# Kernel tuning notes

Hardware: AMD Instinct MI355X
Metric: run time of the kernel (lower is better)

The kernel has to match this reference:

```python
import jax, jax.numpy as jnp
import numpy as np

NUM_HEADS = 16
KEY_SIZE = 64
HEAD_SIZE = 64


def setup_inputs() -> dict:
    key = jax.random.key(0)
    ks = jax.random.split(key, 8)
    B, S, D = 2, 2048, 1024
    s = 1.0 / np.sqrt(D)
    return {
        "q": jax.random.normal(ks[0], (B, S, D), jnp.float32),
        "k": jax.random.normal(ks[1], (B, S, D), jnp.float32),
        "v": jax.random.normal(ks[2], (B, S, D), jnp.float32),
        "v_mask": jax.random.randint(ks[3], (B, S), 0, 2, jnp.int32),
        "Wq": jax.random.normal(ks[4], (D, NUM_HEADS * KEY_SIZE), jnp.float32) * s,
        "Wk": jax.random.normal(ks[5], (D, NUM_HEADS * KEY_SIZE), jnp.float32) * s,
        "Wv": jax.random.normal(ks[6], (D, NUM_HEADS * HEAD_SIZE), jnp.float32) * s,
    }


def reference(q, k, v, v_mask, Wq, Wk, Wv):
    B, Sq, _ = q.shape
    Sk = k.shape[1]
    # projections + split heads: [B, S, H, d]
    qw = (q @ Wq).reshape(B, Sq, NUM_HEADS, KEY_SIZE)
    kw = (k @ Wk).reshape(B, Sk, NUM_HEADS, KEY_SIZE)
    vw = (v @ Wv).reshape(B, Sk, NUM_HEADS, HEAD_SIZE)
    # scores [B, H, Sq, Sk]
    a = jnp.einsum('bqhd,bkhd->bhqk', qw, kw) / np.sqrt(KEY_SIZE).astype(np.float32)
    # additive mask over key axis: x*m - (1-m)*1e12
    m = v_mask.astype(a.dtype)[:, None, None, :]
    a = a * m - (1.0 - m) * 1e12
    a = jax.nn.softmax(a, axis=-1)
    # output [B, Sq, H*head_size]
    o = jnp.einsum('bhqk,bkhd->bqhd', a, vw)
    return o.reshape(B, Sq, NUM_HEADS * HEAD_SIZE)
```

## Files before the change

kernel.cpp:

```cpp
#include <hip/hip_runtime.h>
#include <hip/hip_bf16.h>


#define SEQ 2048
#define DIM 1024
#define NPROJ 1024

typedef __bf16 bf16x8 __attribute__((ext_vector_type(8)));
typedef float floatx4 __attribute__((ext_vector_type(4)));
typedef float floatx16 __attribute__((ext_vector_type(16)));

__device__ inline unsigned short f2bf_bits(float x) {
  __hip_bfloat16 h = __float2bfloat16(x);
  return __builtin_bit_cast(unsigned short, h);
}

__device__ __forceinline__ void gload_lds16(const void* g, void* l) {
  __builtin_amdgcn_global_load_lds((const __attribute__((address_space(1))) void*)g,
                                   (__attribute__((address_space(3))) void*)l, 16, 0, 0);
}

__global__ __launch_bounds__(256) void cvt_x(
    const float* __restrict__ q, const float* __restrict__ k, const float* __restrict__ v,
    unsigned short* __restrict__ xb)
{
  const float* X = blockIdx.z == 0 ? q : (blockIdx.z == 1 ? k : v);
  unsigned short* O = xb + (size_t)blockIdx.z * 4096 * 1024;
  int i0 = blockIdx.x * 256 + threadIdx.x;
  #pragma unroll
  for (int it = 0; it < 4; ++it) {
    int i = i0 + it * 262144;
    float4 f = *reinterpret_cast<const float4*>(&X[(size_t)i * 4]);
    ushort4 o;
    o.x = f2bf_bits(f.x); o.y = f2bf_bits(f.y);
    o.z = f2bf_bits(f.z); o.w = f2bf_bits(f.w);
    *reinterpret_cast<ushort4*>(&O[(size_t)i * 4]) = o;
  }
}

__global__ __launch_bounds__(256) void transpose_w(
    const float* __restrict__ Wq, const float* __restrict__ Wk, const float* __restrict__ Wv,
    unsigned short* __restrict__ WqT, unsigned short* __restrict__ WkT, unsigned short* __restrict__ WvT)
{
  const float* W = blockIdx.z == 0 ? Wq : (blockIdx.z == 1 ? Wk : Wv);
  unsigned short* WT = blockIdx.z == 0 ? WqT : (blockIdx.z == 1 ? WkT : WvT);
  const float sc = (blockIdx.z == 0) ? 0.1803368801f : 1.0f;
  __shared__ float tile[64][65];
  const int k0 = blockIdx.x * 64;
  const int n0 = blockIdx.y * 64;
  const int t = threadIdx.x;
  #pragma unroll
  for (int it = 0; it < 4; ++it) {
    int idx = t + (it << 8);
    int r = idx >> 4, c4 = (idx & 15) << 2;
    float4 v = *reinterpret_cast<const float4*>(&W[(k0 + r) * DIM + n0 + c4]);
    tile[r][c4 + 0] = v.x; tile[r][c4 + 1] = v.y;
    tile[r][c4 + 2] = v.z; tile[r][c4 + 3] = v.w;
  }
  __syncthreads();
  #pragma unroll
  for (int it = 0; it < 4; ++it) {
    int idx = t + (it << 8);
    int r = idx >> 4, c4 = (idx & 15) << 2;
    ushort4 o;
    o.x = f2bf_bits(tile[c4 + 0][r] * sc);
    o.y = f2bf_bits(tile[c4 + 1][r] * sc);
    o.z = f2bf_bits(tile[c4 + 2][r] * sc);
    o.w = f2bf_bits(tile[c4 + 3][r] * sc);
    *reinterpret_cast<ushort4*>(&WT[(n0 + r) * DIM + k0 + c4]) = o;
  }
}

__global__ __launch_bounds__(256, 4) void proj_gemm(
    const unsigned short* __restrict__ xb,
    const unsigned short* __restrict__ WqT, const unsigned short* __restrict__ WkT,
    const unsigned short* __restrict__ WvT,
    unsigned short* __restrict__ qw, unsigned short* __restrict__ kw, unsigned short* __restrict__ vw)
{
  const unsigned short* X = xb + (size_t)blockIdx.z * 4096 * 1024;
  const unsigned short* WT = blockIdx.z == 0 ? WqT : (blockIdx.z == 1 ? WkT : WvT);
  unsigned short* Y = blockIdx.z == 0 ? qw : (blockIdx.z == 1 ? kw : vw);

  __shared__ unsigned short Al[2][128 * 32];
  __shared__ unsigned short Bl[2][128 * 32];

  const int m0 = blockIdx.x * 128, n0 = blockIdx.y * 128;
  const int t = threadIdx.x;
  const int lane = t & 63;
  const int wid = t >> 6;
  const int wm = (wid >> 1) << 6, wn = (wid & 1) << 6;
  const int qd = lane >> 4, ln = lane & 15;

  auto stage = [&](int ks, int bi) {
    const int kb = ks << 6;
    #pragma unroll
    for (int i = 0; i < 2; ++i) {
      int p = t + (i << 8);
      int r = p >> 2, c = p & 3;
      int f = (r + (r >> 2)) & 3;
      gload_lds16((const char*)X + (size_t)(m0 + r) * 2048 + kb + ((c ^ f) << 4),
                  (char*)&Al[bi][0] + p * 16);
      gload_lds16((const char*)WT + (size_t)(n0 + r) * 2048 + kb + ((c ^ f) << 4),
                  (char*)&Bl[bi][0] + p * 16);
    }
  };

  floatx4 acc[4][4] = {};
  stage(0, 0);

  for (int ks = 0; ks < 32; ++ks) {
    __syncthreads();
    if (ks + 1 < 32) stage(ks + 1, (ks + 1) & 1);
    const int bi = ks & 1;
    bf16x8 af[4], bfr[4];
    #pragma unroll
    for (int mb = 0; mb < 4; ++mb) {
      int m = wm + mb * 16 + ln;
      int fm = (m + (m >> 2)) & 3;
      af[mb] = *reinterpret_cast<const bf16x8*>(&Al[bi][m * 32 + ((qd ^ fm) << 3)]);
    }
    #pragma unroll
    for (int nb = 0; nb < 4; ++nb) {
      int n = wn + nb * 16 + ln;
      int fn = (n + (n >> 2)) & 3;
      bfr[nb] = *reinterpret_cast<const bf16x8*>(&Bl[bi][n * 32 + ((qd ^ fn) << 3)]);
    }
    #pragma unroll
    for (int mb = 0; mb < 4; ++mb)
      #pragma unroll
      for (int nb = 0; nb < 4; ++nb)
        acc[mb][nb] = __builtin_amdgcn_mfma_f32_16x16x32_bf16(af[mb], bfr[nb], acc[mb][nb], 0, 0, 0);
  }
  #pragma unroll
  for (int mb = 0; mb < 4; ++mb)
    #pragma unroll
    for (int nb = 0; nb < 4; ++nb)
      #pragma unroll
      for (int i = 0; i < 4; ++i) {
        int m = m0 + wm + mb * 16 + qd * 4 + i;
        int n = n0 + wn + nb * 16 + ln;
        Y[(size_t)m * NPROJ + n] = f2bf_bits(acc[mb][nb][i]);
      }
}

__global__ __launch_bounds__(256) void transpose_v(
    const unsigned short* __restrict__ vw, const int* __restrict__ vmask,
    unsigned short* __restrict__ vt, unsigned short* __restrict__ mb)
{
  if (blockIdx.y == 0 && blockIdx.x < 16) {
    int i = blockIdx.x * 256 + threadIdx.x;
    mb[i] = vmask[i] ? 0x3F80 : 0;
  }
  __shared__ unsigned short tile[64 * 64];
  const int t = threadIdx.x;
  const int s0 = blockIdx.x * 64;
  const int bh = blockIdx.y;
  const int b = bh >> 4, h = bh & 15;
  #pragma unroll
  for (int it = 0; it < 2; ++it) {
    int p = t + (it << 8);
    int s = p >> 3, c = p & 7;
    int cp = (c + (s >> 3) + (s & 7)) & 7;
    int4 d = *reinterpret_cast<const int4*>(&vw[(size_t)(b * SEQ + s0 + s) * NPROJ + h * 64 + c * 8]);
    if (vmask[b * SEQ + s0 + s] == 0) { d.x = 0; d.y = 0; d.z = 0; d.w = 0; }
    *reinterpret_cast<int4*>(&tile[s * 64 + cp * 8]) = d;
  }
  __syncthreads();
  #pragma unroll
  for (int it = 0; it < 2; ++it) {
    int d = (t >> 3) + (it << 5), sc = t & 7;
    struct { alignas(16) unsigned short u[8]; } o;
    #pragma unroll
    for (int j = 0; j < 8; ++j) {
      int s = sc * 8 + j;
      int cp = ((d >> 3) + (s >> 3) + (s & 7)) & 7;
      o.u[j] = tile[s * 64 + cp * 8 + (d & 7)];
    }
    *reinterpret_cast<int4*>(&vt[(size_t)(bh * 64 + d) * SEQ + s0 + sc * 8]) =
        *reinterpret_cast<const int4*>(o.u);
  }
}

__global__ __launch_bounds__(256, 2) void attn_fwd(
    const unsigned short* __restrict__ qw, const unsigned short* __restrict__ kw,
    const unsigned short* __restrict__ vt, const unsigned short* __restrict__ mb,
    float* __restrict__ out)
{
  extern __shared__ char smem[];
  unsigned short* Kl = (unsigned short*)smem;
  unsigned short* Vl = (unsigned short*)(smem + 16384);
  unsigned short* Ml = (unsigned short*)(smem + 32768);

  const int t = threadIdx.x, lane = t & 63, wid = t >> 6;
  const int l5 = lane & 31, hi = lane >> 5;
  const int bh = blockIdx.x;
  const int q0 = blockIdx.y * 128;
  const int b = bh >> 4, h = bh & 15;
  const int base = b * SEQ;
  const int wq = wid * 32;

  auto stage = [&](int kt, int bi) {
    const int k0 = kt << 6;
    #pragma unroll
    for (int i = 0; i < 2; ++i) {
      int rb = wid * 16 + i * 8;
      int r = rb + (lane >> 3);
      int rsrc = (r & ~12) | ((r & 4) << 1) | ((r & 8) >> 1);
      int sw = ((lane & 7) ^ (r & 7)) << 4;
      gload_lds16((const char*)kw + ((size_t)((base + k0 + rsrc) * NPROJ + h * 64) << 1) + sw,
                  (char*)&Kl[bi * 4096] + rb * 128);
      gload_lds16((const char*)vt + ((size_t)((bh * 64 + r) * SEQ + k0) << 1) + sw,
                  (char*)&Vl[bi * 4096] + rb * 128);
    }
    if (wid == 3 && lane < 8)
      gload_lds16((const char*)mb + ((size_t)(base + k0 + lane * 8) << 1), (char*)&Ml[bi * 64]);
  };

  bf16x8 qf[4];
  {
    const unsigned short* qptr =
        qw + (size_t)(base + q0 + wq + l5) * NPROJ + h * 64 + hi * 8;
    #pragma unroll
    for (int kk = 0; kk < 4; ++kk)
      qf[kk] = *reinterpret_cast<const bf16x8*>(qptr + kk * 16);
  }

  floatx16 oa0 = {}, oa1 = {}, la = {};
  stage(0, 0);

  #pragma unroll 2
  for (int kt = 0; kt < SEQ / 64; ++kt) {
    __syncthreads();
    if (kt + 1 < SEQ / 64) stage(kt + 1, (kt + 1) & 1);
    const int bi = kt & 1;

    floatx16 s0 = {}, s1 = {};
    #pragma unroll
    for (int kk = 0; kk < 4; ++kk) {
      int ph = ((kk * 2 + hi) ^ (l5 & 7)) << 3;
      bf16x8 k0f = *reinterpret_cast<const bf16x8*>(&Kl[bi * 4096 + l5 * 64 + ph]);
      bf16x8 k1f = *reinterpret_cast<const bf16x8*>(&Kl[bi * 4096 + (32 + l5) * 64 + ph]);
      s0 = __builtin_amdgcn_mfma_f32_32x32x16_bf16(k0f, qf[kk], s0, 0, 0, 0);
      s1 = __builtin_amdgcn_mfma_f32_32x32x16_bf16(k1f, qf[kk], s1, 0, 0, 0);
    }

    float pe[32];
    #pragma unroll
    for (int r = 0; r < 16; ++r) {
      pe[r]      = __builtin_amdgcn_exp2f(s0[r]);
      pe[16 + r] = __builtin_amdgcn_exp2f(s1[r]);
    }

    #pragma unroll
    for (int kk = 0; kk < 4; ++kk) {
      struct alignas(16) { unsigned short u[8]; } pk;
      #pragma unroll
      for (int j = 0; j < 8; ++j) pk.u[j] = f2bf_bits(pe[8 * kk + j]);
      bf16x8 pa = __builtin_bit_cast(bf16x8, pk);
      int ph = ((kk * 2 + hi) ^ (l5 & 7)) << 3;
      bf16x8 v0 = *reinterpret_cast<const bf16x8*>(&Vl[bi * 4096 + l5 * 64 + ph]);
      bf16x8 v1 = *reinterpret_cast<const bf16x8*>(&Vl[bi * 4096 + (32 + l5) * 64 + ph]);
      bf16x8 mf = *reinterpret_cast<const bf16x8*>(&Ml[bi * 64 + kk * 16 + hi * 8]);
      oa0 = __builtin_amdgcn_mfma_f32_32x32x16_bf16(pa, v0, oa0, 0, 0, 0);
      oa1 = __builtin_amdgcn_mfma_f32_32x32x16_bf16(pa, v1, oa1, 0, 0, 0);
      la  = __builtin_amdgcn_mfma_f32_32x32x16_bf16(pa, mf, la, 0, 0, 0);
    }
  }

  #pragma unroll
  for (int r = 0; r < 16; ++r) {
    int row = wq + (r & 3) + ((r >> 2) << 3) + (hi << 2);
    float inv = 1.0f / la[r];
    size_t o = (size_t)(base + q0 + row) * NPROJ + h * 64;
    out[o + l5] = oa0[r] * inv;
    out[o + 32 + l5] = oa1[r] * inv;
  }
}

extern "C" void kernel_launch(void* const* d_in, const int* in_sizes, int n_in,
                              void* d_out, int out_size, void* d_ws, size_t ws_size,
                              hipStream_t stream) {
  const float* q  = (const float*)d_in[0];
  const float* k  = (const float*)d_in[1];
  const float* v  = (const float*)d_in[2];
  const int* vm   = (const int*)d_in[3];
  const float* Wq = (const float*)d_in[4];
  const float* Wk = (const float*)d_in[5];
  const float* Wv = (const float*)d_in[6];
  float* out = (float*)d_out;

  unsigned short* ws = (unsigned short*)d_ws;
  unsigned short* WqT = ws + ((size_t)0 << 20);
  unsigned short* WkT = ws + ((size_t)1 << 20);
  unsigned short* WvT = ws + ((size_t)2 << 20);
  unsigned short* qw  = ws + ((size_t)3 << 20);
  unsigned short* kw  = ws + ((size_t)7 << 20);
  unsigned short* vw  = ws + ((size_t)11 << 20);
  unsigned short* xb  = ws + ((size_t)15 << 20);
  unsigned short* vt  = ws + ((size_t)15 << 20);
  unsigned short* mbv = WqT;

  cvt_x<<<dim3(1024, 1, 3), 256, 0, stream>>>(q, k, v, xb);
  transpose_w<<<dim3(16, 16, 3), 256, 0, stream>>>(Wq, Wk, Wv, WqT, WkT, WvT);
  proj_gemm<<<dim3(32, 8, 3), 256, 0, stream>>>(xb, WqT, WkT, WvT, qw, kw, vw);
  transpose_v<<<dim3(32, 32), 256, 0, stream>>>(vw, vm, vt, mbv);
  attn_fwd<<<dim3(32, 16), 256, 33024, stream>>>(qw, kw, vt, mbv, out);
}
```

Before: 101.4 us.

## Split key tiles across wave pairs in attention with LDS merge of partial outputs

The attention kernel grows from 4 to 8 waves per block. Each pair of waves shares a 32-query slice and splits each 64-key tile in half, computing half the scores and PV MFMAs per wave. Partial outputs and row sums are combined through shared memory at the end. s_setprio hints are added around the MFMA sections. This raises wave-level parallelism and latency hiding, at the cost of duplicated Q fragments, a final LDS reduction, and more register and occupancy pressure.

```diff
diff --git a/kernel.cpp b/kernel.cpp
--- a/kernel.cpp
+++ b/kernel.cpp
@@ -181,7 +181,7 @@
   }
 }
 
-__global__ __launch_bounds__(256, 2) void attn_fwd(
+__global__ __launch_bounds__(512, 4) void attn_fwd(
     const unsigned short* __restrict__ qw, const unsigned short* __restrict__ kw,
     const unsigned short* __restrict__ vt, const unsigned short* __restrict__ mb,
     float* __restrict__ out)
@@ -193,33 +193,30 @@
 
   const int t = threadIdx.x, lane = t & 63, wid = t >> 6;
   const int l5 = lane & 31, hi = lane >> 5;
+  const int qh = wid >> 1, kh = wid & 1;
   const int bh = blockIdx.x;
   const int q0 = blockIdx.y * 128;
   const int b = bh >> 4, h = bh & 15;
   const int base = b * SEQ;
-  const int wq = wid * 32;
 
   auto stage = [&](int kt, int bi) {
     const int k0 = kt << 6;
-    #pragma unroll
-    for (int i = 0; i < 2; ++i) {
-      int rb = wid * 16 + i * 8;
-      int r = rb + (lane >> 3);
-      int rsrc = (r & ~12) | ((r & 4) << 1) | ((r & 8) >> 1);
-      int sw = ((lane & 7) ^ (r & 7)) << 4;
-      gload_lds16((const char*)kw + ((size_t)((base + k0 + rsrc) * NPROJ + h * 64) << 1) + sw,
-                  (char*)&Kl[bi * 4096] + rb * 128);
-      gload_lds16((const char*)vt + ((size_t)((bh * 64 + r) * SEQ + k0) << 1) + sw,
-                  (char*)&Vl[bi * 4096] + rb * 128);
-    }
-    if (wid == 3 && lane < 8)
+    int rb = wid * 8;
+    int r = rb + (lane >> 3);
+    int rsrc = (r & ~12) | ((r & 4) << 1) | ((r & 8) >> 1);
+    int sw = ((lane & 7) ^ (r & 7)) << 4;
+    gload_lds16((const char*)kw + ((size_t)((base + k0 + rsrc) * NPROJ + h * 64) << 1) + sw,
+                (char*)&Kl[bi * 4096] + rb * 128);
+    gload_lds16((const char*)vt + ((size_t)((bh * 64 + r) * SEQ + k0) << 1) + sw,
+                (char*)&Vl[bi * 4096] + rb * 128);
+    if (wid == 7 && lane < 8)
       gload_lds16((const char*)mb + ((size_t)(base + k0 + lane * 8) << 1), (char*)&Ml[bi * 64]);
   };
 
   bf16x8 qf[4];
   {
     const unsigned short* qptr =
-        qw + (size_t)(base + q0 + wq + l5) * NPROJ + h * 64 + hi * 8;
+        qw + (size_t)(base + q0 + qh * 32 + l5) * NPROJ + h * 64 + hi * 8;
     #pragma unroll
     for (int kk = 0; kk < 4; ++kk)
       qf[kk] = *reinterpret_cast<const bf16x8*>(qptr + kk * 16);
@@ -234,46 +231,61 @@
     if (kt + 1 < SEQ / 64) stage(kt + 1, (kt + 1) & 1);
     const int bi = kt & 1;
 
-    floatx16 s0 = {}, s1 = {};
+    floatx16 s = {};
+    __builtin_amdgcn_s_setprio(1);
     #pragma unroll
     for (int kk = 0; kk < 4; ++kk) {
       int ph = ((kk * 2 + hi) ^ (l5 & 7)) << 3;
-      bf16x8 k0f = *reinterpret_cast<const bf16x8*>(&Kl[bi * 4096 + l5 * 64 + ph]);
-      bf16x8 k1f = *reinterpret_cast<const bf16x8*>(&Kl[bi * 4096 + (32 + l5) * 64 + ph]);
-      s0 = __builtin_amdgcn_mfma_f32_32x32x16_bf16(k0f, qf[kk], s0, 0, 0, 0);
-      s1 = __builtin_amdgcn_mfma_f32_32x32x16_bf16(k1f, qf[kk], s1, 0, 0, 0);
-    }
-
-    float pe[32];
-    #pragma unroll
-    for (int r = 0; r < 16; ++r) {
-      pe[r]      = __builtin_amdgcn_exp2f(s0[r]);
-      pe[16 + r] = __builtin_amdgcn_exp2f(s1[r]);
-    }
-
-    #pragma unroll
-    for (int kk = 0; kk < 4; ++kk) {
+      bf16x8 kf = *reinterpret_cast<const bf16x8*>(&Kl[bi * 4096 + (kh * 32 + l5) * 64 + ph]);
+      s = __builtin_amdgcn_mfma_f32_32x32x16_bf16(kf, qf[kk], s, 0, 0, 0);
+    }
+    __builtin_amdgcn_s_setprio(0);
+
+    float pe[16];
+    #pragma unroll
+    for (int r = 0; r < 16; ++r) pe[r] = __builtin_amdgcn_exp2f(s[r]);
+
+    #pragma unroll
+    for (int kk = 0; kk < 2; ++kk) {
       struct alignas(16) { unsigned short u[8]; } pk;
       #pragma unroll
       for (int j = 0; j < 8; ++j) pk.u[j] = f2bf_bits(pe[8 * kk + j]);
       bf16x8 pa = __builtin_bit_cast(bf16x8, pk);
-      int ph = ((kk * 2 + hi) ^ (l5 & 7)) << 3;
-      bf16x8 v0 = *reinterpret_cast<const bf16x8*>(&Vl[bi * 4096 + l5 * 64 + ph]);
-      bf16x8 v1 = *reinterpret_cast<const bf16x8*>(&Vl[bi * 4096 + (32 + l5) * 64 + ph]);
-      bf16x8 mf = *reinterpret_cast<const bf16x8*>(&Ml[bi * 64 + kk * 16 + hi * 8]);
+      int ch = ((4 * kh + 2 * kk + hi) ^ (l5 & 7)) << 3;
+      bf16x8 v0 = *reinterpret_cast<const bf16x8*>(&Vl[bi * 4096 + l5 * 64 + ch]);
+      bf16x8 v1 = *reinterpret_cast<const bf16x8*>(&Vl[bi * 4096 + (32 + l5) * 64 + ch]);
+      bf16x8 mf = *reinterpret_cast<const bf16x8*>(&Ml[bi * 64 + kh * 32 + kk * 16 + hi * 8]);
+      __builtin_amdgcn_s_setprio(1);
       oa0 = __builtin_amdgcn_mfma_f32_32x32x16_bf16(pa, v0, oa0, 0, 0, 0);
       oa1 = __builtin_amdgcn_mfma_f32_32x32x16_bf16(pa, v1, oa1, 0, 0, 0);
       la  = __builtin_amdgcn_mfma_f32_32x32x16_bf16(pa, mf, la, 0, 0, 0);
-    }
-  }
-
-  #pragma unroll
-  for (int r = 0; r < 16; ++r) {
-    int row = wq + (r & 3) + ((r >> 2) << 3) + (hi << 2);
-    float inv = 1.0f / la[r];
-    size_t o = (size_t)(base + q0 + row) * NPROJ + h * 64;
-    out[o + l5] = oa0[r] * inv;
-    out[o + 32 + l5] = oa1[r] * inv;
+      __builtin_amdgcn_s_setprio(0);
+    }
+  }
+
+  __syncthreads();
+  float* Mg = (float*)smem;
+  if (kh == 1) {
+    #pragma unroll
+    for (int r = 0; r < 16; ++r) {
+      int row = qh * 32 + (r & 3) + ((r >> 2) << 3) + (hi << 2);
+      Mg[row * 66 + l5] = oa0[r];
+      Mg[row * 66 + 32 + l5] = oa1[r];
+      if (l5 == 0) Mg[row * 66 + 64] = la[r];
+    }
+  }
+  __syncthreads();
+  if (kh == 0) {
+    #pragma unroll
+    for (int r = 0; r < 16; ++r) {
+      int row = qh * 32 + (r & 3) + ((r >> 2) << 3) + (hi << 2);
+      float o0 = oa0[r] + Mg[row * 66 + l5];
+      float o1 = oa1[r] + Mg[row * 66 + 32 + l5];
+      float inv = 1.0f / (la[r] + Mg[row * 66 + 64]);
+      size_t o = (size_t)(base + q0 + row) * NPROJ + h * 64;
+      out[o + l5] = o0 * inv;
+      out[o + 32 + l5] = o1 * inv;
+    }
   }
 }
 
@@ -304,5 +316,5 @@
   transpose_w<<<dim3(16, 16, 3), 256, 0, stream>>>(Wq, Wk, Wv, WqT, WkT, WvT);
   proj_gemm<<<dim3(32, 8, 3), 256, 0, stream>>>(xb, WqT, WkT, WvT, qw, kw, vw);
   transpose_v<<<dim3(32, 32), 256, 0, stream>>>(vw, vm, vt, mbv);
-  attn_fwd<<<dim3(32, 16), 256, 33024, stream>>>(qw, kw, vt, mbv, out);
-}
+  attn_fwd<<<dim3(32, 16), 512, 33792, stream>>>(qw, kw, vt, mbv, out);
+}
```

Result: no change. 102.9 us (+1.4%).
